# Kernel optimization log

Measured on AMD Instinct MI355X. Metric: run time of the kernel, lower is better.

The kernel has to match this reference:

```python
import math
import jax, jax.numpy as jnp
import numpy as np

ALPHA = 0.1   # label_smoothing_factor
BLANK = 0     # blank_id
NEG = -1e9    # safe -inf for fp32 log-space DP


def setup_inputs() -> dict:
    key = jax.random.key(0)
    k1, k2, k3, k4 = jax.random.split(key, 4)
    N, T, U, C = 4, 256, 64, 1024
    logits = jax.random.normal(k1, (N, T, U + 1, C), dtype=jnp.float32)
    targets = jax.random.randint(k2, (N, U), 1, C, dtype=jnp.int32)
    x_lens = jax.random.randint(k3, (N,), T // 2, T + 1, dtype=jnp.int32)
    y_lens = jax.random.randint(k4, (N,), U // 2, U + 1, dtype=jnp.int32)
    return {"logits": logits, "targets": targets, "x_lens": x_lens, "y_lens": y_lens}


def _reverse_label_smoothing(logprobs, alpha):
    # logprobs*(1-a) + sum(logprobs)*(a/C) + target_entropy
    C = logprobs.shape[-1]
    target_entropy = -((1.0 - alpha) * math.log(1.0 - alpha)
                       + alpha * math.log(alpha / C))
    s = jnp.sum(logprobs, axis=-1, keepdims=True)
    return logprobs * (1.0 - alpha) + s * (alpha / C) + target_entropy


def _rnnt_loss(log_probs, targets, x_lens, y_lens):
    # log_probs: (N, T, U1, C); standard RNN-T forward algorithm, sum reduction
    N, T, U1, C = log_probs.shape
    blank_lp = log_probs[..., BLANK]                      # (N, T, U1)
    idx = jnp.pad(targets, ((0, 0), (0, 1)))              # (N, U1), pad col unused
    emit = jnp.take_along_axis(
        log_probs,
        jnp.broadcast_to(idx[:, None, :, None].astype(jnp.int32), (N, T, U1, 1)),
        axis=3)[..., 0]                                   # (N, T, U1)

    def row(a, emit_row):
        # alpha[t,u] = logaddexp(a[u], alpha[t,u-1] + emit[t,u-1]); scan over u
        def step(c, xs):
            a_u, e_u = xs
            v = jnp.logaddexp(a_u, c)
            return v + e_u, v
        _, vals = jax.lax.scan(step, jnp.full((N,), NEG, log_probs.dtype),
                               (a.T, emit_row.T))
        return vals.T                                     # (N, U1)

    a0 = jnp.full((N, U1), NEG, log_probs.dtype).at[:, 0].set(0.0)
    alpha0 = row(a0, emit[:, 0])                          # t = 0 row

    def t_step(alpha_prev, xs):
        blank_prev, emit_row = xs
        alpha_t = row(alpha_prev + blank_prev, emit_row)
        return alpha_t, alpha_t

    xs = (jnp.moveaxis(blank_lp[:, :-1], 1, 0),           # (T-1, N, U1)
          jnp.moveaxis(emit[:, 1:], 1, 0))
    _, alphas_rest = jax.lax.scan(t_step, alpha0, xs)
    alphas = jnp.concatenate([alpha0[None], alphas_rest], axis=0)  # (T, N, U1)

    n = jnp.arange(N)
    final = alphas[x_lens - 1, n, y_lens] + blank_lp[n, x_lens - 1, y_lens]
    return -jnp.sum(final)


def reference(logits, targets, x_lens, y_lens):
    lp = jax.nn.log_softmax(logits, axis=-1)
    lp = _reverse_label_smoothing(lp, ALPHA)
    return _rnnt_loss(lp, targets, x_lens, y_lens)
```

## Files before the change

### kernel.cpp

```cpp
#include <hip/hip_runtime.h>
#include <math.h>

constexpr int N = 4, T = 256, U = 64, U1 = 65, C = 1024;
constexpr float ALPHA = 0.1f;
constexpr float NEG = -1e9f;
constexpr float TE = 1.01823015f;
constexpr float INV_LN2 = 1.4426950408889634f;
constexpr float LN2 = 0.6931471805599453f;

constexpr int NCH = 40;
constexpr size_t UPV_F = (size_t)N * NCH * 64 * 8;
constexpr size_t LFV_F = UPV_F;
constexpr size_t BLK0_F = (size_t)N * NCH * 8;

__device__ __forceinline__ void process_row(
    int r, int lane, float4 v0, float4 v1, float4 v2, float4 v3,
    const int* __restrict__ targets, const int* __restrict__ x_lens,
    const int* __restrict__ y_lens,
    float* __restrict__ upv, float* __restrict__ lfv,
    float* __restrict__ blk0, float* __restrict__ blankFinal) {
  int n = r / (T * U1);
  int rem = r - n * (T * U1);
  int t = rem / U1;
  int u = rem - t * U1;

  float s = ((v0.x + v0.y) + (v0.z + v0.w)) + ((v1.x + v1.y) + (v1.z + v1.w))
          + ((v2.x + v2.y) + (v2.z + v2.w)) + ((v3.x + v3.y) + (v3.z + v3.w));
  float z = exp2f(v0.x * INV_LN2) + exp2f(v0.y * INV_LN2)
          + exp2f(v0.z * INV_LN2) + exp2f(v0.w * INV_LN2)
          + exp2f(v1.x * INV_LN2) + exp2f(v1.y * INV_LN2)
          + exp2f(v1.z * INV_LN2) + exp2f(v1.w * INV_LN2)
          + exp2f(v2.x * INV_LN2) + exp2f(v2.y * INV_LN2)
          + exp2f(v2.z * INV_LN2) + exp2f(v2.w * INV_LN2)
          + exp2f(v3.x * INV_LN2) + exp2f(v3.y * INV_LN2)
          + exp2f(v3.z * INV_LN2) + exp2f(v3.w * INV_LN2);
  #pragma unroll
  for (int off = 1; off < 64; off <<= 1) {
    s += __shfl_xor(s, off);
    z += __shfl_xor(z, off);
  }

  float lse2 = __log2f(z);
  float coef = (s * INV_LN2 - (float)C * lse2) * (ALPHA / (float)C) + TE * INV_LN2;

  if (lane == 0) {
    float bval = (v0.x * INV_LN2 - lse2) * (1.0f - ALPHA) + coef;
    int i = t + u;
    if (u >= 1) upv[((size_t)(n * NCH + (i >> 3)) * 64 + (u - 1)) * 8 + (i & 7)] = bval;
    else        blk0[((size_t)(n * NCH) + (t >> 3)) * 8 + (t & 7)] = bval;
    if (t == x_lens[n] - 1 && u == y_lens[n]) blankFinal[n] = bval;
  }
  if (u < U) {
    int tgt = targets[n * U + u];
    if (lane == ((tgt >> 2) & 63)) {
      int k = tgt >> 8, j = tgt & 3;
      float4 vk = (k == 0) ? v0 : (k == 1) ? v1 : (k == 2) ? v2 : v3;
      float xv = (j == 0) ? vk.x : (j == 1) ? vk.y : (j == 2) ? vk.z : vk.w;
      float ev = (xv * INV_LN2 - lse2) * (1.0f - ALPHA) + coef;
      int i = t + u;
      lfv[((size_t)(n * NCH + (i >> 3)) * 64 + u) * 8 + (i & 7)] = ev;
    }
  }
}

__global__ __launch_bounds__(256) void row_reduce_kernel(
    const float* __restrict__ logits, const int* __restrict__ targets,
    const int* __restrict__ x_lens, const int* __restrict__ y_lens,
    float* __restrict__ upv, float* __restrict__ lfv,
    float* __restrict__ blk0, float* __restrict__ blankFinal) {
  int w = blockIdx.x * 4 + (threadIdx.x >> 6);
  int lane = threadIdx.x & 63;
  int r0 = 2 * w, r1 = r0 + 1;
  const float4* x0 = reinterpret_cast<const float4*>(logits + (size_t)r0 * C);
  const float4* x1 = reinterpret_cast<const float4*>(logits + (size_t)r1 * C);
  float4 a0 = x0[lane], a1 = x0[64 + lane], a2 = x0[128 + lane], a3 = x0[192 + lane];
  float4 b0 = x1[lane], b1 = x1[64 + lane], b2 = x1[128 + lane], b3 = x1[192 + lane];
  process_row(r0, lane, a0, a1, a2, a3, targets, x_lens, y_lens, upv, lfv, blk0, blankFinal);
  process_row(r1, lane, b0, b1, b2, b3, targets, x_lens, y_lens, upv, lfv, blk0, blankFinal);
}

__global__ __launch_bounds__(256) void dp_kernel(
    const float* __restrict__ upv, const float* __restrict__ lfv,
    const float* __restrict__ blk0, const float* __restrict__ blankFinal,
    const int* __restrict__ x_lens, const int* __restrict__ y_lens,
    float* __restrict__ out) {
  __shared__ float part[N];
  int tid = threadIdx.x;
  int n = tid >> 6, lane = tid & 63;
  int u = lane + 1;
  int xl = x_lens[n], yl = y_lens[n];
  int dfin = (xl - 1) + yl;
  int clast = (dfin - 1) >> 3;

  const float4* upB = reinterpret_cast<const float4*>(upv);
  const float4* lfB = reinterpret_cast<const float4*>(lfv);
  const float4* b0B = reinterpret_cast<const float4*>(blk0);
  size_t ubase = ((size_t)(n * NCH) * 64 + lane) * 2;

  float aprev = NEG;
  float a0 = 0.0f;
  float aFinal = 0.0f;

  float4 uA0 = upB[ubase],           uA1 = upB[ubase + 1];
  float4 lA0 = lfB[ubase],           lA1 = lfB[ubase + 1];
  float4 zA0 = b0B[(size_t)n * NCH * 2], zA1 = b0B[(size_t)n * NCH * 2 + 1];

  for (int c = 0; c <= clast; ++c) {
    int cn = (c < clast) ? c + 1 : c;
    float4 uB0 = upB[ubase + (size_t)cn * 128];
    float4 uB1 = upB[ubase + (size_t)cn * 128 + 1];
    float4 lB0 = lfB[ubase + (size_t)cn * 128];
    float4 lB1 = lfB[ubase + (size_t)cn * 128 + 1];
    float4 zB0 = b0B[((size_t)n * NCH + cn) * 2];
    float4 zB1 = b0B[((size_t)n * NCH + cn) * 2 + 1];

    int dbase = 8 * c + 1;
#define DP_STEP(UP, LF, B0, J)                                           \
    {                                                                    \
      int d = dbase + (J);                                               \
      float ln = __shfl_up(aprev, 1);                                    \
      if (u == 1) ln = a0;                                               \
      float xup = aprev + (UP);                                          \
      float left = ln + (LF);                                            \
      float mm = fmaxf(xup, left);                                       \
      float val = mm + __log2f(1.0f + exp2f(-fabsf(xup - left)));        \
      aprev = val;                                                       \
      if (d == dfin && u == yl) aFinal = val;                            \
      a0 += (B0);                                                        \
    }
    DP_STEP(uA0.x, lA0.x, zA0.x, 0)
    DP_STEP(uA0.y, lA0.y, zA0.y, 1)
    DP_STEP(uA0.z, lA0.z, zA0.z, 2)
    DP_STEP(uA0.w, lA0.w, zA0.w, 3)
    DP_STEP(uA1.x, lA1.x, zA1.x, 4)
    DP_STEP(uA1.y, lA1.y, zA1.y, 5)
    DP_STEP(uA1.z, lA1.z, zA1.z, 6)
    DP_STEP(uA1.w, lA1.w, zA1.w, 7)
#undef DP_STEP
    uA0 = uB0; uA1 = uB1; lA0 = lB0; lA1 = lB1; zA0 = zB0; zA1 = zB1;
  }

  if (u == yl) part[n] = aFinal + blankFinal[n];
  __syncthreads();
  if (tid == 0)
    out[0] = -((part[0] + part[1]) + (part[2] + part[3])) * LN2;
}

extern "C" void kernel_launch(void* const* d_in, const int* in_sizes, int n_in,
                              void* d_out, int out_size, void* d_ws, size_t ws_size,
                              hipStream_t stream) {
  const float* logits  = (const float*)d_in[0];
  const int*   targets = (const int*)d_in[1];
  const int*   x_lens  = (const int*)d_in[2];
  const int*   y_lens  = (const int*)d_in[3];
  float* out = (float*)d_out;

  float* upv        = (float*)d_ws;
  float* lfv        = upv + UPV_F;
  float* blk0       = lfv + LFV_F;
  float* blankFinal = blk0 + BLK0_F;

  int nrows = N * T * U1;
  row_reduce_kernel<<<dim3(nrows / 8), dim3(256), 0, stream>>>(
      logits, targets, x_lens, y_lens, upv, lfv, blk0, blankFinal);
  dp_kernel<<<dim3(1), dim3(256), 0, stream>>>(
      upv, lfv, blk0, blankFinal, x_lens, y_lens, out);
}
```

Measured before the change: 71.27 us.

## Use persistent-style waves with software-prefetched nontemporal row loads

The row-reduce kernel now launches far fewer blocks, and each wave processes 16 rows strided across the grid instead of 2 adjacent rows. The next row's data is loaded before the current one is processed, so one row's load latency overlaps the previous row's reductions. Loads use nontemporal hints to avoid polluting the cache with streamed logits. The trade-off is lower parallelism per launch and higher register pressure from the double-buffered row data.

```diff
diff --git a/kernel.cpp b/kernel.cpp
--- a/kernel.cpp
+++ b/kernel.cpp
@@ -12,9 +12,15 @@
 constexpr size_t UPV_F = (size_t)N * NCH * 64 * 8;
 constexpr size_t LFV_F = UPV_F;
 constexpr size_t BLK0_F = (size_t)N * NCH * 8;
+constexpr int NROWS = N * T * U1;
+constexpr int RPW = 16;
+constexpr int NWAVE = NROWS / RPW;
+constexpr int NBLK = NWAVE / 4;
+
+typedef float v4f __attribute__((ext_vector_type(4)));
 
 __device__ __forceinline__ void process_row(
-    int r, int lane, float4 v0, float4 v1, float4 v2, float4 v3,
+    int r, int lane, v4f v0, v4f v1, v4f v2, v4f v3,
     const int* __restrict__ targets, const int* __restrict__ x_lens,
     const int* __restrict__ y_lens,
     float* __restrict__ upv, float* __restrict__ lfv,
@@ -54,7 +60,7 @@
     int tgt = targets[n * U + u];
     if (lane == ((tgt >> 2) & 63)) {
       int k = tgt >> 8, j = tgt & 3;
-      float4 vk = (k == 0) ? v0 : (k == 1) ? v1 : (k == 2) ? v2 : v3;
+      v4f vk = (k == 0) ? v0 : (k == 1) ? v1 : (k == 2) ? v2 : v3;
       float xv = (j == 0) ? vk.x : (j == 1) ? vk.y : (j == 2) ? vk.z : vk.w;
       float ev = (xv * INV_LN2 - lse2) * (1.0f - ALPHA) + coef;
       int i = t + u;
@@ -68,15 +74,30 @@
     const int* __restrict__ x_lens, const int* __restrict__ y_lens,
     float* __restrict__ upv, float* __restrict__ lfv,
     float* __restrict__ blk0, float* __restrict__ blankFinal) {
-  int w = blockIdx.x * 4 + (threadIdx.x >> 6);
+  int wid = blockIdx.x * 4 + (threadIdx.x >> 6);
   int lane = threadIdx.x & 63;
-  int r0 = 2 * w, r1 = r0 + 1;
-  const float4* x0 = reinterpret_cast<const float4*>(logits + (size_t)r0 * C);
-  const float4* x1 = reinterpret_cast<const float4*>(logits + (size_t)r1 * C);
-  float4 a0 = x0[lane], a1 = x0[64 + lane], a2 = x0[128 + lane], a3 = x0[192 + lane];
-  float4 b0 = x1[lane], b1 = x1[64 + lane], b2 = x1[128 + lane], b3 = x1[192 + lane];
-  process_row(r0, lane, a0, a1, a2, a3, targets, x_lens, y_lens, upv, lfv, blk0, blankFinal);
-  process_row(r1, lane, b0, b1, b2, b3, targets, x_lens, y_lens, upv, lfv, blk0, blankFinal);
+  const v4f* base = reinterpret_cast<const v4f*>(logits);
+
+  size_t p = (size_t)wid * 256 + lane;
+  v4f c0 = __builtin_nontemporal_load(base + p);
+  v4f c1 = __builtin_nontemporal_load(base + p + 64);
+  v4f c2 = __builtin_nontemporal_load(base + p + 128);
+  v4f c3 = __builtin_nontemporal_load(base + p + 192);
+
+  for (int i = 0; i < RPW; ++i) {
+    int r = wid + NWAVE * i;
+    v4f n0 = c0, n1 = c1, n2 = c2, n3 = c3;
+    if (i + 1 < RPW) {
+      size_t q = (size_t)(r + NWAVE) * 256 + lane;
+      n0 = __builtin_nontemporal_load(base + q);
+      n1 = __builtin_nontemporal_load(base + q + 64);
+      n2 = __builtin_nontemporal_load(base + q + 128);
+      n3 = __builtin_nontemporal_load(base + q + 192);
+    }
+    process_row(r, lane, c0, c1, c2, c3, targets, x_lens, y_lens,
+                upv, lfv, blk0, blankFinal);
+    c0 = n0; c1 = n1; c2 = n2; c3 = n3;
+  }
 }
 
 __global__ __launch_bounds__(256) void dp_kernel(
@@ -92,27 +113,27 @@
   int dfin = (xl - 1) + yl;
   int clast = (dfin - 1) >> 3;
 
-  const float4* upB = reinterpret_cast<const float4*>(upv);
-  const float4* lfB = reinterpret_cast<const float4*>(lfv);
-  const float4* b0B = reinterpret_cast<const float4*>(blk0);
+  const v4f* upB = reinterpret_cast<const v4f*>(upv);
+  const v4f* lfB = reinterpret_cast<const v4f*>(lfv);
+  const v4f* b0B = reinterpret_cast<const v4f*>(blk0);
   size_t ubase = ((size_t)(n * NCH) * 64 + lane) * 2;
 
   float aprev = NEG;
   float a0 = 0.0f;
   float aFinal = 0.0f;
 
-  float4 uA0 = upB[ubase],           uA1 = upB[ubase + 1];
-  float4 lA0 = lfB[ubase],           lA1 = lfB[ubase + 1];
-  float4 zA0 = b0B[(size_t)n * NCH * 2], zA1 = b0B[(size_t)n * NCH * 2 + 1];
+  v4f uA0 = upB[ubase],               uA1 = upB[ubase + 1];
+  v4f lA0 = lfB[ubase],               lA1 = lfB[ubase + 1];
+  v4f zA0 = b0B[(size_t)n * NCH * 2], zA1 = b0B[(size_t)n * NCH * 2 + 1];
 
   for (int c = 0; c <= clast; ++c) {
     int cn = (c < clast) ? c + 1 : c;
-    float4 uB0 = upB[ubase + (size_t)cn * 128];
-    float4 uB1 = upB[ubase + (size_t)cn * 128 + 1];
-    float4 lB0 = lfB[ubase + (size_t)cn * 128];
-    float4 lB1 = lfB[ubase + (size_t)cn * 128 + 1];
-    float4 zB0 = b0B[((size_t)n * NCH + cn) * 2];
-    float4 zB1 = b0B[((size_t)n * NCH + cn) * 2 + 1];
+    v4f uB0 = upB[ubase + (size_t)cn * 128];
+    v4f uB1 = upB[ubase + (size_t)cn * 128 + 1];
+    v4f lB0 = lfB[ubase + (size_t)cn * 128];
+    v4f lB1 = lfB[ubase + (size_t)cn * 128 + 1];
+    v4f zB0 = b0B[((size_t)n * NCH + cn) * 2];
+    v4f zB1 = b0B[((size_t)n * NCH + cn) * 2 + 1];
 
     int dbase = 8 * c + 1;
 #define DP_STEP(UP, LF, B0, J)                                           \
@@ -160,8 +181,7 @@
   float* blk0       = lfv + LFV_F;
   float* blankFinal = blk0 + BLK0_F;
 
-  int nrows = N * T * U1;
-  row_reduce_kernel<<<dim3(nrows / 8), dim3(256), 0, stream>>>(
+  row_reduce_kernel<<<dim3(NBLK), dim3(256), 0, stream>>>(
       logits, targets, x_lens, y_lens, upv, lfv, blk0, blankFinal);
   dp_kernel<<<dim3(1), dim3(256), 0, stream>>>(
       upv, lfv, blk0, blankFinal, x_lens, y_lens, out);
```

Result: slower. 79.18 us (+11.1%).
